# Kernel optimization log

Hardware: AMD Instinct MI355X
Metric: run time of the kernel (lower is better)

## Reference

```python
import jax, jax.numpy as jnp
from jax import lax
import numpy as np

NUM_HEADS = 8
KW = 3  # window kernel size

def _avgpool3(x):
    # x: [B,C,H,W]; AvgPool2d(3,1,1) with count_include_pad=True -> sum/9
    s = lax.reduce_window(x, 0.0, lax.add, (1, 1, KW, KW), (1, 1, 1, 1),
                          ((0, 0), (0, 0), (1, 1), (1, 1)))
    return s / (KW * KW)

def _unfold3(y):
    # y: [B,h,w,C] -> [B,h,w,9,C]; patch index ordered row-major (kh,kw)
    B, h, w, C = y.shape
    yp = jnp.pad(y, ((0, 0), (1, 1), (1, 1), (0, 0)))
    return jnp.stack([yp[:, i:i + h, j:j + w, :]
                      for i in range(KW) for j in range(KW)], axis=3)

def setup_inputs():
    key = jax.random.key(0)
    ks = jax.random.split(key, 9)
    B, C, H, W = 8, 256, 64, 64
    sd = 0.02
    return {
        "x": jax.random.normal(ks[0], (B, C, H, W), jnp.float32),
        "W_qkv": jax.random.normal(ks[1], (4 * C, C), jnp.float32) * sd,
        "b_qkv": jnp.zeros((4 * C,), jnp.float32),
        "W1": jax.random.normal(ks[2], (C // 2, C), jnp.float32) * sd,
        "b1": jnp.zeros((C // 2,), jnp.float32),
        "W2": jax.random.normal(ks[3], (C, C // 2), jnp.float32) * sd,
        "b2": jnp.zeros((C,), jnp.float32),
        "Wp": jax.random.normal(ks[4], (C, C), jnp.float32) * sd,
        "bp": jnp.zeros((C,), jnp.float32),
    }

def reference(x, W_qkv, b_qkv, W1, b1, W2, b2, Wp, bp):
    B, C, H, W = x.shape
    nH = NUM_HEADS
    hd = C // nH
    scale = hd ** -0.5
    # avg pool (stride 1 keeps spatial dims), to channels-last
    y = _avgpool3(x).transpose(0, 2, 3, 1)                 # [B,h,w,C]
    qkv = y @ W_qkv.T + b_qkv                              # [B,h,w,4C]
    qkv = qkv.reshape(B, H, W, C, 4)
    q, k, v, chans = qkv[..., 0], qkv[..., 1], qkv[..., 2], qkv[..., 3]
    # channel gate
    g = jax.nn.sigmoid(jax.nn.relu(chans @ W1.T + b1) @ W2.T + b2)  # [B,h,w,C]
    # local window attention: each query attends to its 3x3 neighborhood
    qh = q.reshape(B, H, W, nH, hd)                        # [B,h,w,n,d]
    kp = _unfold3(k).reshape(B, H, W, KW * KW, nH, hd)     # [B,h,w,9,n,d]
    vp = _unfold3(v).reshape(B, H, W, KW * KW, nH, hd)
    attn = jnp.einsum('bhwnd,bhwknd->bhwnk', qh, kp) * scale
    attn = jax.nn.softmax(attn, axis=-1)
    out = jnp.einsum('bhwnk,bhwknd->bhwnd', attn, vp).reshape(B, H, W, C)
    out = out * g + out
    out = out @ Wp.T + bp
    return out.transpose(0, 3, 1, 2)                       # [B,C,H,W]
```

## Files before the change

kernel.cpp:

```cpp
#include <hip/hip_runtime.h>
#include <stdint.h>

typedef __bf16    bf16x8 __attribute__((ext_vector_type(8)));
typedef float     f32x4  __attribute__((ext_vector_type(4)));
typedef uint32_t  u32x4  __attribute__((ext_vector_type(4)));

#define MFMA(a,b,c) __builtin_amdgcn_mfma_f32_16x16x32_bf16((a),(b),(c),0,0,0)

__device__ __align__(16) uint16_t g_y [8*64*64*256];
__device__ __align__(16) uint16_t g_wpk[393216];

#define WQF 0
#define WKF 65536
#define WVF 131072
#define WCF 196608
#define W1F 262144
#define W2F 294912
#define WPF 327680

static __device__ __forceinline__ float b2f(uint32_t u){ return __builtin_bit_cast(float, u<<16); }
static __device__ __forceinline__ uint32_t f2b(float f){
  uint32_t x = __builtin_bit_cast(uint32_t, f);
  return (x + 0x7fffu + ((x>>16)&1u)) >> 16;
}

__global__ __launch_bounds__(256) void kpack(const float* __restrict__ Wqkv,
    const float* __restrict__ W1, const float* __restrict__ W2,
    const float* __restrict__ Wp){
  int idx = blockIdx.x*256 + threadIdx.x;
  int j = idx & 7, lane = (idx>>3)&63;
  int n16 = lane & 15, q4 = lane>>4;
  float v;
  if (idx < 262144){
    int t = idx >> 16, l = idx & 65535;
    int s = (l>>9)&7, nt = l>>12;
    v = Wqkv[(4*(nt*16+n16) + t)*256 + s*32 + q4*8 + j];
  } else if (idx < 294912){
    int l = idx - 262144;
    int s = (l>>9)&7, nt = l>>12;
    v = W1[(nt*16+n16)*256 + s*32 + q4*8 + j];
  } else if (idx < 327680){
    int l = idx - 294912;
    int s = (l>>9)&3, nt = l>>11;
    v = W2[(nt*16+n16)*128 + s*32 + q4*8 + j];
  } else {
    int l = idx - 327680;
    int s = (l>>9)&7, nt = l>>12;
    v = Wp[(nt*16+n16)*256 + s*32 + q4*8 + j];
  }
  g_wpk[idx] = (uint16_t)f2b(v);
}

__global__ __launch_bounds__(512) void kpool(const float* __restrict__ x){
  __shared__ __align__(16) uint16_t sm[3*256*82];
  uint32_t* smw = (uint32_t*)sm;
  int t = threadIdx.x;
  int b = blockIdx.x >> 6, h = blockIdx.x & 63;
  for (int i=t; i<768; i+=512){
    int base = i*41;
    smw[base+3]  = 0;
    smw[base+36] = 0;
  }
  if (h==0 || h==63){
    int hh = (h==0) ? 0 : 2;
    for (int i=t; i<10496; i+=512) smw[hh*10496 + i] = 0;
  }
  #pragma unroll
  for (int i=0;i<24;i++){
    int id = t + 512*i;
    int w4 = id&15, c = (id>>4)&255, hh = id>>12;
    int gy = h - 1 + hh;
    if ((unsigned)gy < 64u){
      f32x4 ld = *(const f32x4*)&x[(((b*256+c)*64+gy)*64) + w4*4];
      int wb = (((hh*256+c)*82 + 8 + w4*4) >> 1);
      smw[wb+0] = f2b(ld[0]) | (f2b(ld[1])<<16);
      smw[wb+1] = f2b(ld[2]) | (f2b(ld[3])<<16);
    }
  }
  __syncthreads();
  int c = t & 255, wsel = t >> 8;
  int r0 = c*82, r1 = r0 + 256*82, r2 = r1 + 256*82;
  int w0 = wsel*32;
  float csp = b2f(sm[r0+w0+7]) + b2f(sm[r1+w0+7]) + b2f(sm[r2+w0+7]);
  float csc = b2f(sm[r0+w0+8]) + b2f(sm[r1+w0+8]) + b2f(sm[r2+w0+8]);
  uint16_t* dst = g_y + ((b*64+h)*64)*256 + c;
  for (int j2=0;j2<32;j2++){
    int w = w0 + j2;
    float csn = b2f(sm[r0+w+9]) + b2f(sm[r1+w+9]) + b2f(sm[r2+w+9]);
    float yv = (csp + csc + csn) * (1.0f/9.0f);
    dst[w*256] = (uint16_t)f2b(yv);
    csp = csc; csc = csn;
  }
}

#define YSTR 264
#define HSTR 134
#define K2_QS 26400
#define K2_KS 34976
#define K2_VS 48376
#define MCH 0
#define MHS 16896
#define MAO 25600
__global__ __launch_bounds__(512,2) void kattn(const float* __restrict__ bqkv,
    const float* __restrict__ b1, const float* __restrict__ b2v,
    const float* __restrict__ bp, float* __restrict__ out){
  __shared__ __align__(16) uint16_t sm[61776];
  int t = threadIdx.x;
  int lane = t & 63, wave = t >> 6;
  int n16 = lane & 15, quad = lane >> 4;
  int bid = blockIdx.x;
  int bb = bid>>6, tyhi=(bid>>4)&3, txl=(bid>>3)&1, tylo=(bid>>2)&1, txp=bid&3;
  int ty = tyhi*2+tylo, tx = txp*2+txl;

  uint32_t opk[2][16];
  uint32_t chp[32];

  #pragma unroll
  for (int i=0;i<7;i++){
    int id = t + 512*i;
    if (id < 3200){
      int hp = id >> 5, c8 = id & 31;
      int py = hp/10, px = hp - py*10;
      int gy = ty*8 + py - 1, gx = tx*8 + px - 1;
      u32x4 ld = {0,0,0,0};
      if ((unsigned)gy<64u && (unsigned)gx<64u)
        ld = *(const u32x4*)&g_y[((bb*64+gy)*64+gx)*256 + c8*8];
      *(u32x4*)&sm[hp*YSTR + c8*8] = ld;
    }
  }
  __syncthreads();

  #pragma unroll
  for (int hf=0; hf<2; hf++){
    {
      int ntg = hf*8 + wave;
      bf16x8 Bq[8];
      #pragma unroll
      for (int s=0;s<8;s++) Bq[s] = *(const bf16x8*)&g_wpk[WQF + ((ntg*8+s)*64+lane)*8];
      float bq = bqkv[4*(ntg*16+n16) + 0];
      int colB = wave*16;
      #pragma unroll
      for (int mt=0; mt<4; mt++){
        f32x4 a = {0.f,0.f,0.f,0.f};
        int m = mt*16 + n16;
        int hrow = 10*(m>>3) + (m&7) + 11;
        #pragma unroll
        for (int s=0;s<8;s++){
          bf16x8 A = *(const bf16x8*)&sm[hrow*YSTR + s*32 + quad*8];
          a = MFMA(A, Bq[s], a);
        }
        #pragma unroll
        for (int r=0;r<4;r++){
          int row = mt*16 + quad*4 + r;
          sm[K2_QS + row*HSTR + colB + n16] = (uint16_t)f2b(a[r] + bq);
        }
      }
    }
    __syncthreads();
    {
      int ntg = hf*8 + wave;
      bf16x8 Bk[8], Bv[8];
      #pragma unroll
      for (int s=0;s<8;s++){
        Bk[s] = *(const bf16x8*)&g_wpk[WKF + ((ntg*8+s)*64+lane)*8];
        Bv[s] = *(const bf16x8*)&g_wpk[WVF + ((ntg*8+s)*64+lane)*8];
      }
      float bk = bqkv[4*(ntg*16+n16) + 1];
      float bv = bqkv[4*(ntg*16+n16) + 2];
      int colB = wave*16;
      #pragma unroll
      for (int mt=0; mt<7; mt++){
        f32x4 ak = {0.f,0.f,0.f,0.f}, av = {0.f,0.f,0.f,0.f};
        int m = mt*16 + n16;
        int mr = (m < 100) ? m : 99;
        #pragma unroll
        for (int s=0;s<8;s++){
          bf16x8 A = *(const bf16x8*)&sm[mr*YSTR + s*32 + quad*8];
          ak = MFMA(A, Bk[s], ak);
          av = MFMA(A, Bv[s], av);
        }
        #pragma unroll
        for (int r=0;r<4;r++){
          int row = mt*16 + quad*4 + r;
          if (row < 100){
            int py = row/10, px = row - py*10;
            int gy = ty*8 + py - 1, gx = tx*8 + px - 1;
            bool ok = ((unsigned)gy<64u) && ((unsigned)gx<64u);
            float vk = ok ? ak[r] + bk : 0.f;
            float vv = ok ? av[r] + bv : 0.f;
            sm[K2_KS + row*HSTR + colB + n16] = (uint16_t)f2b(vk);
            sm[K2_VS + row*HSTR + colB + n16] = (uint16_t)f2b(vv);
          }
        }
      }
    }
    __syncthreads();
    if (wave < 4){
      int p = t & 63, hl = wave;
      int iy = p >> 3, ix = p & 7;
      int cb = hl*32;
      const uint32_t* q32 = (const uint32_t*)&sm[K2_QS + p*HSTR + cb];
      float qv[32];
      #pragma unroll
      for (int i=0;i<16;i++){ uint32_t u=q32[i]; qv[2*i]=b2f(u&0xffffu); qv[2*i+1]=b2f(u>>16); }
      int hb = (iy+1)*10 + ix + 1;
      const int off[9] = {-11,-10,-9,-1,0,1,9,10,11};
      float sc[9];
      #pragma unroll
      for (int nb=0;nb<9;nb++){
        const uint32_t* k32 = (const uint32_t*)&sm[K2_KS + (hb+off[nb])*HSTR + cb];
        float s = 0.f;
        #pragma unroll
        for (int i=0;i<16;i++){ uint32_t u=k32[i]; s += qv[2*i]*b2f(u&0xffffu) + qv[2*i+1]*b2f(u>>16); }
        sc[nb] = s * 0.17677669529663687f;
      }
      float mx = sc[0];
      #pragma unroll
      for (int nb=1;nb<9;nb++) mx = fmaxf(mx, sc[nb]);
      float l = 0.f;
      #pragma unroll
      for (int nb=0;nb<9;nb++){ sc[nb] = __expf(sc[nb]-mx); l += sc[nb]; }
      float inv = 1.f / l;
      float o[32];
      #pragma unroll
      for (int i=0;i<32;i++) o[i]=0.f;
      #pragma unroll
      for (int nb=0;nb<9;nb++){
        float wgt = sc[nb]*inv;
        const uint32_t* v32 = (const uint32_t*)&sm[K2_VS + (hb+off[nb])*HSTR + cb];
        #pragma unroll
        for (int i=0;i<16;i++){ uint32_t u=v32[i]; o[2*i] += wgt*b2f(u&0xffffu); o[2*i+1] += wgt*b2f(u>>16); }
      }
      #pragma unroll
      for (int i=0;i<16;i++) opk[hf][i] = f2b(o[2*i]) | (f2b(o[2*i+1])<<16);
    } else if (hf == 0){
      #pragma unroll
      for (int jj=0;jj<4;jj++){
        int ntg = (wave-4)*4 + jj;
        bf16x8 Bc[8];
        #pragma unroll
        for (int s=0;s<8;s++) Bc[s] = *(const bf16x8*)&g_wpk[WCF + ((ntg*8+s)*64+lane)*8];
        float bc = bqkv[4*(ntg*16+n16) + 3];
        #pragma unroll
        for (int mt=0; mt<4; mt++){
          f32x4 a = {0.f,0.f,0.f,0.f};
          int m = mt*16 + n16;
          int hrow = 10*(m>>3) + (m&7) + 11;
          #pragma unroll
          for (int s=0;s<8;s++){
            bf16x8 A = *(const bf16x8*)&sm[hrow*YSTR + s*32 + quad*8];
            a = MFMA(A, Bc[s], a);
          }
          chp[(jj*4+mt)*2+0] = f2b(a[0]+bc) | (f2b(a[1]+bc)<<16);
          chp[(jj*4+mt)*2+1] = f2b(a[2]+bc) | (f2b(a[3]+bc)<<16);
        }
      }
    } else {
      #pragma unroll
      for (int jj=0;jj<4;jj++){
        int ntg = (wave-4)*4 + jj;
        int col = ntg*16 + n16;
        #pragma unroll
        for (int mt=0;mt<4;mt++){
          #pragma unroll
          for (int r2=0;r2<2;r2++){
            uint32_t v = chp[(jj*4+mt)*2+r2];
            int row = mt*16 + quad*4 + r2*2;
            sm[MCH + row*264 + col]     = (uint16_t)(v & 0xffffu);
            sm[MCH + (row+1)*264 + col] = (uint16_t)(v >> 16);
          }
        }
      }
    }
    __syncthreads();
  }
  if (wave < 4){
    int p = t & 63, cb = wave*32;
    #pragma unroll
    for (int hf=0;hf<2;hf++)
      #pragma unroll
      for (int i=0;i<16;i++)
        *(uint32_t*)&sm[MAO + p*264 + hf*128 + cb + 2*i] = opk[hf][i];
  }
  {
    int ntg = wave;
    bf16x8 Bf[8];
    #pragma unroll
    for (int s=0;s<8;s++) Bf[s] = *(const bf16x8*)&g_wpk[W1F + ((ntg*8+s)*64+lane)*8];
    float bs = b1[ntg*16+n16];
    int colB = wave*16;
    #pragma unroll
    for (int mt=0;mt<4;mt++){
      f32x4 a = {0.f,0.f,0.f,0.f};
      #pragma unroll
      for (int s=0;s<8;s++){
        bf16x8 A = *(const bf16x8*)&sm[MCH + (mt*16+n16)*264 + s*32 + quad*8];
        a = MFMA(A, Bf[s], a);
      }
      #pragma unroll
      for (int r=0;r<4;r++){
        int row = mt*16 + quad*4 + r;
        sm[MHS + row*136 + colB + n16] = (uint16_t)f2b(fmaxf(a[r]+bs, 0.f));
      }
    }
  }
  __syncthreads();
  #pragma unroll
  for (int jj=0;jj<2;jj++){
    int ntg = wave*2 + jj;
    bf16x8 Bf[4];
    #pragma unroll
    for (int s=0;s<4;s++) Bf[s] = *(const bf16x8*)&g_wpk[W2F + ((ntg*4+s)*64+lane)*8];
    float bs = b2v[ntg*16+n16];
    int colB = ntg*16;
    #pragma unroll
    for (int mt=0;mt<4;mt++){
      f32x4 a = {0.f,0.f,0.f,0.f};
      #pragma unroll
      for (int s=0;s<4;s++){
        bf16x8 A = *(const bf16x8*)&sm[MHS + (mt*16+n16)*136 + s*32 + quad*8];
        a = MFMA(A, Bf[s], a);
      }
      #pragma unroll
      for (int r=0;r<4;r++){
        int row = mt*16 + quad*4 + r;
        float gg = 1.f/(1.f+__expf(-(a[r] + bs)));
        float ao = b2f((uint32_t)sm[MAO + row*264 + colB + n16]);
        sm[MCH + row*264 + colB + n16] = (uint16_t)f2b(ao*(1.f+gg));
      }
    }
  }
  __syncthreads();
  #pragma unroll
  for (int jj=0;jj<2;jj++){
    int ntg = wave*2 + jj;
    bf16x8 Bf[8];
    #pragma unroll
    for (int s=0;s<8;s++) Bf[s] = *(const bf16x8*)&g_wpk[WPF + ((ntg*8+s)*64+lane)*8];
    float bs = bp[ntg*16+n16];
    int colB = ntg*16;
    #pragma unroll
    for (int mt=0;mt<4;mt++){
      f32x4 a = {0.f,0.f,0.f,0.f};
      #pragma unroll
      for (int s=0;s<8;s++){
        bf16x8 A = *(const bf16x8*)&sm[MCH + (mt*16+n16)*264 + s*32 + quad*8];
        a = MFMA(A, Bf[s], a);
      }
      #pragma unroll
      for (int r=0;r<4;r++){
        int row = mt*16 + quad*4 + r;
        sm[MAO + row*264 + colB + n16] = (uint16_t)f2b(a[r]+bs);
      }
    }
  }
  __syncthreads();
  #pragma unroll
  for (int i=0;i<8;i++){
    int idx = t + 512*i;
    int ix4 = idx&1, iy = (idx>>1)&7, c = idx>>4;
    f32x4 stv;
    #pragma unroll
    for (int j=0;j<4;j++){
      int p = iy*8 + ix4*4 + j;
      stv[j] = b2f((uint32_t)sm[MAO + p*264 + c]);
    }
    *(f32x4*)&out[(((bb*256+c)*64) + ty*8+iy)*64 + tx*8 + ix4*4] = stv;
  }
}

extern "C" void kernel_launch(void* const* d_in, const int* in_sizes, int n_in,
                              void* d_out, int out_size, void* d_ws, size_t ws_size,
                              hipStream_t stream){
  (void)in_sizes; (void)n_in; (void)d_ws; (void)ws_size; (void)out_size;
  const float* x    = (const float*)d_in[0];
  const float* Wqkv = (const float*)d_in[1];
  const float* bqkv = (const float*)d_in[2];
  const float* W1   = (const float*)d_in[3];
  const float* b1   = (const float*)d_in[4];
  const float* W2   = (const float*)d_in[5];
  const float* b2   = (const float*)d_in[6];
  const float* Wp   = (const float*)d_in[7];
  const float* bp   = (const float*)d_in[8];
  kpack<<<dim3(1536), dim3(256), 0, stream>>>(Wqkv, W1, W2, Wp);
  kpool<<<dim3(512),  dim3(512), 0, stream>>>(x);
  kattn<<<dim3(512),  dim3(512), 0, stream>>>(bqkv, b1, b2, bp, (float*)d_out);
}
```

Before: 190.5 us.

## Merge pack and pool kernels, halve attention tile to 8x4 for occupancy

Fuses weight packing and average pooling into one launch, with pooling split into half-channel blocks. The attention kernel tile shrinks from 8x8 to 4x8 pixels, which shrinks the shared memory footprint and register arrays and raises the launch-bounds target from 2 to 4 blocks per CU over 1024 blocks. Each attention thread now covers half a head's channels and combines partial dot products with a cross-lane shuffle, and shared-memory strides are padded to reduce bank conflicts. The smaller tile raises halo overhead: 60 halo rows per 32 outputs instead of 100 per 64, so more redundant K/V projection work.

```diff
diff --git a/kernel.cpp b/kernel.cpp
--- a/kernel.cpp
+++ b/kernel.cpp
@@ -24,104 +24,105 @@
   return (x + 0x7fffu + ((x>>16)&1u)) >> 16;
 }
 
-__global__ __launch_bounds__(256) void kpack(const float* __restrict__ Wqkv,
-    const float* __restrict__ W1, const float* __restrict__ W2,
-    const float* __restrict__ Wp){
-  int idx = blockIdx.x*256 + threadIdx.x;
-  int j = idx & 7, lane = (idx>>3)&63;
-  int n16 = lane & 15, q4 = lane>>4;
-  float v;
-  if (idx < 262144){
-    int t = idx >> 16, l = idx & 65535;
-    int s = (l>>9)&7, nt = l>>12;
-    v = Wqkv[(4*(nt*16+n16) + t)*256 + s*32 + q4*8 + j];
-  } else if (idx < 294912){
-    int l = idx - 262144;
-    int s = (l>>9)&7, nt = l>>12;
-    v = W1[(nt*16+n16)*256 + s*32 + q4*8 + j];
-  } else if (idx < 327680){
-    int l = idx - 294912;
-    int s = (l>>9)&3, nt = l>>11;
-    v = W2[(nt*16+n16)*128 + s*32 + q4*8 + j];
+__global__ __launch_bounds__(512) void kprep(const float* __restrict__ x,
+    const float* __restrict__ Wqkv, const float* __restrict__ W1,
+    const float* __restrict__ W2, const float* __restrict__ Wp){
+  int t = threadIdx.x;
+  int bid = blockIdx.x;
+  if (bid < 1024){
+    __shared__ __align__(16) uint16_t sm[3*128*82];
+    uint32_t* smw = (uint32_t*)sm;
+    int b = bid >> 7, h = (bid >> 1) & 63, ch = (bid & 1) << 7;
+    for (int i=t; i<384; i+=512){
+      int base = i*41;
+      smw[base+3]  = 0;
+      smw[base+36] = 0;
+    }
+    if (h==0 || h==63){
+      int hh = (h==0) ? 0 : 2;
+      for (int i=t; i<5248; i+=512) smw[hh*5248 + i] = 0;
+    }
+    #pragma unroll
+    for (int i=0;i<12;i++){
+      int id = t + 512*i;
+      int w4 = id&15, c = (id>>4)&127, hh = id>>11;
+      int gy = h - 1 + hh;
+      if ((unsigned)gy < 64u){
+        f32x4 ld = *(const f32x4*)&x[(((b*256+ch+c)*64+gy)*64) + w4*4];
+        int wb = (((hh*128+c)*82 + 8 + w4*4) >> 1);
+        smw[wb+0] = f2b(ld[0]) | (f2b(ld[1])<<16);
+        smw[wb+1] = f2b(ld[2]) | (f2b(ld[3])<<16);
+      }
+    }
+    __syncthreads();
+    int c = t & 127, wsel = t >> 7;
+    int r0 = c*82, r1 = r0 + 128*82, r2 = r1 + 128*82;
+    int w0 = wsel*16;
+    float csp = b2f(sm[r0+w0+7]) + b2f(sm[r1+w0+7]) + b2f(sm[r2+w0+7]);
+    float csc = b2f(sm[r0+w0+8]) + b2f(sm[r1+w0+8]) + b2f(sm[r2+w0+8]);
+    uint16_t* dst = g_y + ((b*64+h)*64)*256 + ch + c;
+    for (int j2=0;j2<16;j2++){
+      int w = w0 + j2;
+      float csn = b2f(sm[r0+w+9]) + b2f(sm[r1+w+9]) + b2f(sm[r2+w+9]);
+      float yv = (csp + csc + csn) * (1.0f/9.0f);
+      dst[w*256] = (uint16_t)f2b(yv);
+      csp = csc; csc = csn;
+    }
   } else {
-    int l = idx - 327680;
-    int s = (l>>9)&7, nt = l>>12;
-    v = Wp[(nt*16+n16)*256 + s*32 + q4*8 + j];
-  }
-  g_wpk[idx] = (uint16_t)f2b(v);
+    int idx = (bid - 1024)*512 + t;
+    int j = idx & 7, lane = (idx>>3)&63;
+    int n16 = lane & 15, q4 = lane>>4;
+    float v;
+    if (idx < 262144){
+      int tt = idx >> 16, l = idx & 65535;
+      int s = (l>>9)&7, nt = l>>12;
+      v = Wqkv[(4*(nt*16+n16) + tt)*256 + s*32 + q4*8 + j];
+    } else if (idx < 294912){
+      int l = idx - 262144;
+      int s = (l>>9)&7, nt = l>>12;
+      v = W1[(nt*16+n16)*256 + s*32 + q4*8 + j];
+    } else if (idx < 327680){
+      int l = idx - 294912;
+      int s = (l>>9)&3, nt = l>>11;
+      v = W2[(nt*16+n16)*128 + s*32 + q4*8 + j];
+    } else {
+      int l = idx - 327680;
+      int s = (l>>9)&7, nt = l>>12;
+      v = Wp[(nt*16+n16)*256 + s*32 + q4*8 + j];
+    }
+    g_wpk[idx] = (uint16_t)f2b(v);
+  }
 }
 
-__global__ __launch_bounds__(512) void kpool(const float* __restrict__ x){
-  __shared__ __align__(16) uint16_t sm[3*256*82];
-  uint32_t* smw = (uint32_t*)sm;
-  int t = threadIdx.x;
-  int b = blockIdx.x >> 6, h = blockIdx.x & 63;
-  for (int i=t; i<768; i+=512){
-    int base = i*41;
-    smw[base+3]  = 0;
-    smw[base+36] = 0;
-  }
-  if (h==0 || h==63){
-    int hh = (h==0) ? 0 : 2;
-    for (int i=t; i<10496; i+=512) smw[hh*10496 + i] = 0;
-  }
-  #pragma unroll
-  for (int i=0;i<24;i++){
-    int id = t + 512*i;
-    int w4 = id&15, c = (id>>4)&255, hh = id>>12;
-    int gy = h - 1 + hh;
-    if ((unsigned)gy < 64u){
-      f32x4 ld = *(const f32x4*)&x[(((b*256+c)*64+gy)*64) + w4*4];
-      int wb = (((hh*256+c)*82 + 8 + w4*4) >> 1);
-      smw[wb+0] = f2b(ld[0]) | (f2b(ld[1])<<16);
-      smw[wb+1] = f2b(ld[2]) | (f2b(ld[3])<<16);
-    }
-  }
-  __syncthreads();
-  int c = t & 255, wsel = t >> 8;
-  int r0 = c*82, r1 = r0 + 256*82, r2 = r1 + 256*82;
-  int w0 = wsel*32;
-  float csp = b2f(sm[r0+w0+7]) + b2f(sm[r1+w0+7]) + b2f(sm[r2+w0+7]);
-  float csc = b2f(sm[r0+w0+8]) + b2f(sm[r1+w0+8]) + b2f(sm[r2+w0+8]);
-  uint16_t* dst = g_y + ((b*64+h)*64)*256 + c;
-  for (int j2=0;j2<32;j2++){
-    int w = w0 + j2;
-    float csn = b2f(sm[r0+w+9]) + b2f(sm[r1+w+9]) + b2f(sm[r2+w+9]);
-    float yv = (csp + csc + csn) * (1.0f/9.0f);
-    dst[w*256] = (uint16_t)f2b(yv);
-    csp = csc; csc = csn;
-  }
-}
-
-#define YSTR 264
-#define HSTR 134
-#define K2_QS 26400
-#define K2_KS 34976
-#define K2_VS 48376
-#define MCH 0
-#define MHS 16896
-#define MAO 25600
-__global__ __launch_bounds__(512,2) void kattn(const float* __restrict__ bqkv,
+#define YSTR  264
+#define HSTR  136
+#define K2_QS 15840
+#define K2_KS 20192
+#define K2_VS 28352
+#define MCH   0
+#define MHS   8448
+#define MAO   15840
+#define MAOSTR 266
+__global__ __launch_bounds__(512,4) void kattn(const float* __restrict__ bqkv,
     const float* __restrict__ b1, const float* __restrict__ b2v,
     const float* __restrict__ bp, float* __restrict__ out){
-  __shared__ __align__(16) uint16_t sm[61776];
+  __shared__ __align__(16) uint16_t sm[36512];
   int t = threadIdx.x;
   int lane = t & 63, wave = t >> 6;
   int n16 = lane & 15, quad = lane >> 4;
   int bid = blockIdx.x;
-  int bb = bid>>6, tyhi=(bid>>4)&3, txl=(bid>>3)&1, tylo=(bid>>2)&1, txp=bid&3;
-  int ty = tyhi*2+tylo, tx = txp*2+txl;
-
-  uint32_t opk[2][16];
-  uint32_t chp[32];
+  int bb = bid >> 7, ty = (bid >> 3) & 15, tx = bid & 7;
+
+  uint32_t opk[2][8];
+  uint32_t chp[16];
 
   #pragma unroll
-  for (int i=0;i<7;i++){
+  for (int i=0;i<4;i++){
     int id = t + 512*i;
-    if (id < 3200){
+    if (id < 1920){
       int hp = id >> 5, c8 = id & 31;
       int py = hp/10, px = hp - py*10;
-      int gy = ty*8 + py - 1, gx = tx*8 + px - 1;
+      int gy = ty*4 + py - 1, gx = tx*8 + px - 1;
       u32x4 ld = {0,0,0,0};
       if ((unsigned)gy<64u && (unsigned)gx<64u)
         ld = *(const u32x4*)&g_y[((bb*64+gy)*64+gx)*256 + c8*8];
@@ -140,7 +141,7 @@
       float bq = bqkv[4*(ntg*16+n16) + 0];
       int colB = wave*16;
       #pragma unroll
-      for (int mt=0; mt<4; mt++){
+      for (int mt=0; mt<2; mt++){
         f32x4 a = {0.f,0.f,0.f,0.f};
         int m = mt*16 + n16;
         int hrow = 10*(m>>3) + (m&7) + 11;
@@ -169,10 +170,10 @@
       float bv = bqkv[4*(ntg*16+n16) + 2];
       int colB = wave*16;
       #pragma unroll
-      for (int mt=0; mt<7; mt++){
+      for (int mt=0; mt<4; mt++){
         f32x4 ak = {0.f,0.f,0.f,0.f}, av = {0.f,0.f,0.f,0.f};
         int m = mt*16 + n16;
-        int mr = (m < 100) ? m : 99;
+        int mr = (m < 60) ? m : 59;
         #pragma unroll
         for (int s=0;s<8;s++){
           bf16x8 A = *(const bf16x8*)&sm[mr*YSTR + s*32 + quad*8];
@@ -182,9 +183,9 @@
         #pragma unroll
         for (int r=0;r<4;r++){
           int row = mt*16 + quad*4 + r;
-          if (row < 100){
+          if (row < 60){
             int py = row/10, px = row - py*10;
-            int gy = ty*8 + py - 1, gx = tx*8 + px - 1;
+            int gy = ty*4 + py - 1, gx = tx*8 + px - 1;
             bool ok = ((unsigned)gy<64u) && ((unsigned)gx<64u);
             float vk = ok ? ak[r] + bk : 0.f;
             float vv = ok ? av[r] + bv : 0.f;
@@ -196,22 +197,32 @@
     }
     __syncthreads();
     if (wave < 4){
-      int p = t & 63, hl = wave;
-      int iy = p >> 3, ix = p & 7;
-      int cb = hl*32;
-      const uint32_t* q32 = (const uint32_t*)&sm[K2_QS + p*HSTR + cb];
-      float qv[32];
-      #pragma unroll
-      for (int i=0;i<16;i++){ uint32_t u=q32[i]; qv[2*i]=b2f(u&0xffffu); qv[2*i+1]=b2f(u>>16); }
-      int hb = (iy+1)*10 + ix + 1;
+      int p = lane & 31, half = lane >> 5;
+      int cb = wave*32 + half*16;
+      const uint16_t* qp = &sm[K2_QS + p*HSTR + cb];
+      u32x4 qa = *(const u32x4*)qp;
+      u32x4 qb = *(const u32x4*)(qp+8);
+      float qv[16];
+      #pragma unroll
+      for (int i=0;i<4;i++){
+        qv[2*i]    = b2f(qa[i]&0xffffu); qv[2*i+1]   = b2f(qa[i]>>16);
+        qv[8+2*i]  = b2f(qb[i]&0xffffu); qv[8+2*i+1] = b2f(qb[i]>>16);
+      }
+      int hb = 10*(p>>3) + (p&7) + 11;
       const int off[9] = {-11,-10,-9,-1,0,1,9,10,11};
       float sc[9];
       #pragma unroll
       for (int nb=0;nb<9;nb++){
-        const uint32_t* k32 = (const uint32_t*)&sm[K2_KS + (hb+off[nb])*HSTR + cb];
+        const uint16_t* kp = &sm[K2_KS + (hb+off[nb])*HSTR + cb];
+        u32x4 ka = *(const u32x4*)kp;
+        u32x4 kb = *(const u32x4*)(kp+8);
         float s = 0.f;
         #pragma unroll
-        for (int i=0;i<16;i++){ uint32_t u=k32[i]; s += qv[2*i]*b2f(u&0xffffu) + qv[2*i+1]*b2f(u>>16); }
+        for (int i=0;i<4;i++){
+          s += qv[2*i]*b2f(ka[i]&0xffffu)   + qv[2*i+1]*b2f(ka[i]>>16);
+          s += qv[8+2*i]*b2f(kb[i]&0xffffu) + qv[8+2*i+1]*b2f(kb[i]>>16);
+        }
+        s += __shfl_xor(s, 32);
         sc[nb] = s * 0.17677669529663687f;
       }
       float mx = sc[0];
@@ -221,18 +232,23 @@
       #pragma unroll
       for (int nb=0;nb<9;nb++){ sc[nb] = __expf(sc[nb]-mx); l += sc[nb]; }
       float inv = 1.f / l;
-      float o[32];
-      #pragma unroll
-      for (int i=0;i<32;i++) o[i]=0.f;
+      float o[16];
+      #pragma unroll
+      for (int i=0;i<16;i++) o[i]=0.f;
       #pragma unroll
       for (int nb=0;nb<9;nb++){
         float wgt = sc[nb]*inv;
-        const uint32_t* v32 = (const uint32_t*)&sm[K2_VS + (hb+off[nb])*HSTR + cb];
-        #pragma unroll
-        for (int i=0;i<16;i++){ uint32_t u=v32[i]; o[2*i] += wgt*b2f(u&0xffffu); o[2*i+1] += wgt*b2f(u>>16); }
-      }
-      #pragma unroll
-      for (int i=0;i<16;i++) opk[hf][i] = f2b(o[2*i]) | (f2b(o[2*i+1])<<16);
+        const uint16_t* vp = &sm[K2_VS + (hb+off[nb])*HSTR + cb];
+        u32x4 va = *(const u32x4*)vp;
+        u32x4 vb = *(const u32x4*)(vp+8);
+        #pragma unroll
+        for (int i=0;i<4;i++){
+          o[2*i]    += wgt*b2f(va[i]&0xffffu); o[2*i+1]   += wgt*b2f(va[i]>>16);
+          o[8+2*i]  += wgt*b2f(vb[i]&0xffffu); o[8+2*i+1] += wgt*b2f(vb[i]>>16);
+        }
+      }
+      #pragma unroll
+      for (int i=0;i<8;i++) opk[hf][i] = f2b(o[2*i]) | (f2b(o[2*i+1])<<16);
     } else if (hf == 0){
       #pragma unroll
       for (int jj=0;jj<4;jj++){
@@ -242,7 +258,7 @@
         for (int s=0;s<8;s++) Bc[s] = *(const bf16x8*)&g_wpk[WCF + ((ntg*8+s)*64+lane)*8];
         float bc = bqkv[4*(ntg*16+n16) + 3];
         #pragma unroll
-        for (int mt=0; mt<4; mt++){
+        for (int mt=0; mt<2; mt++){
           f32x4 a = {0.f,0.f,0.f,0.f};
           int m = mt*16 + n16;
           int hrow = 10*(m>>3) + (m&7) + 11;
@@ -251,8 +267,8 @@
             bf16x8 A = *(const bf16x8*)&sm[hrow*YSTR + s*32 + quad*8];
             a = MFMA(A, Bc[s], a);
           }
-          chp[(jj*4+mt)*2+0] = f2b(a[0]+bc) | (f2b(a[1]+bc)<<16);
-          chp[(jj*4+mt)*2+1] = f2b(a[2]+bc) | (f2b(a[3]+bc)<<16);
+          chp[(jj*2+mt)*2+0] = f2b(a[0]+bc) | (f2b(a[1]+bc)<<16);
+          chp[(jj*2+mt)*2+1] = f2b(a[2]+bc) | (f2b(a[3]+bc)<<16);
         }
       }
     } else {
@@ -261,10 +277,10 @@
         int ntg = (wave-4)*4 + jj;
         int col = ntg*16 + n16;
         #pragma unroll
-        for (int mt=0;mt<4;mt++){
+        for (int mt=0;mt<2;mt++){
           #pragma unroll
           for (int r2=0;r2<2;r2++){
-            uint32_t v = chp[(jj*4+mt)*2+r2];
+            uint32_t v = chp[(jj*2+mt)*2+r2];
             int row = mt*16 + quad*4 + r2*2;
             sm[MCH + row*264 + col]     = (uint16_t)(v & 0xffffu);
             sm[MCH + (row+1)*264 + col] = (uint16_t)(v >> 16);
@@ -275,12 +291,13 @@
     __syncthreads();
   }
   if (wave < 4){
-    int p = t & 63, cb = wave*32;
+    int p = lane & 31, half = lane >> 5;
+    int cb = wave*32 + half*16;
     #pragma unroll
     for (int hf=0;hf<2;hf++)
       #pragma unroll
-      for (int i=0;i<16;i++)
-        *(uint32_t*)&sm[MAO + p*264 + hf*128 + cb + 2*i] = opk[hf][i];
+      for (int i=0;i<8;i++)
+        *(uint32_t*)&sm[MAO + p*MAOSTR + hf*128 + cb + 2*i] = opk[hf][i];
   }
   {
     int ntg = wave;
@@ -290,7 +307,7 @@
     float bs = b1[ntg*16+n16];
     int colB = wave*16;
     #pragma unroll
-    for (int mt=0;mt<4;mt++){
+    for (int mt=0;mt<2;mt++){
       f32x4 a = {0.f,0.f,0.f,0.f};
       #pragma unroll
       for (int s=0;s<8;s++){
@@ -300,7 +317,7 @@
       #pragma unroll
       for (int r=0;r<4;r++){
         int row = mt*16 + quad*4 + r;
-        sm[MHS + row*136 + colB + n16] = (uint16_t)f2b(fmaxf(a[r]+bs, 0.f));
+        sm[MHS + row*HSTR + colB + n16] = (uint16_t)f2b(fmaxf(a[r]+bs, 0.f));
       }
     }
   }
@@ -314,18 +331,18 @@
     float bs = b2v[ntg*16+n16];
     int colB = ntg*16;
     #pragma unroll
-    for (int mt=0;mt<4;mt++){
+    for (int mt=0;mt<2;mt++){
       f32x4 a = {0.f,0.f,0.f,0.f};
       #pragma unroll
       for (int s=0;s<4;s++){
-        bf16x8 A = *(const bf16x8*)&sm[MHS + (mt*16+n16)*136 + s*32 + quad*8];
+        bf16x8 A = *(const bf16x8*)&sm[MHS + (mt*16+n16)*HSTR + s*32 + quad*8];
         a = MFMA(A, Bf[s], a);
       }
       #pragma unroll
       for (int r=0;r<4;r++){
         int row = mt*16 + quad*4 + r;
         float gg = 1.f/(1.f+__expf(-(a[r] + bs)));
-        float ao = b2f((uint32_t)sm[MAO + row*264 + colB + n16]);
+        float ao = b2f((uint32_t)sm[MAO + row*MAOSTR + colB + n16]);
         sm[MCH + row*264 + colB + n16] = (uint16_t)f2b(ao*(1.f+gg));
       }
     }
@@ -340,7 +357,7 @@
     float bs = bp[ntg*16+n16];
     int colB = ntg*16;
     #pragma unroll
-    for (int mt=0;mt<4;mt++){
+    for (int mt=0;mt<2;mt++){
       f32x4 a = {0.f,0.f,0.f,0.f};
       #pragma unroll
       for (int s=0;s<8;s++){
@@ -350,22 +367,22 @@
       #pragma unroll
       for (int r=0;r<4;r++){
         int row = mt*16 + quad*4 + r;
-        sm[MAO + row*264 + colB + n16] = (uint16_t)f2b(a[r]+bs);
+        sm[MAO + row*MAOSTR + colB + n16] = (uint16_t)f2b(a[r]+bs);
       }
     }
   }
   __syncthreads();
   #pragma unroll
-  for (int i=0;i<8;i++){
+  for (int i=0;i<4;i++){
     int idx = t + 512*i;
-    int ix4 = idx&1, iy = (idx>>1)&7, c = idx>>4;
+    int ix4 = idx&1, iy = (idx>>1)&3, c = idx>>3;
     f32x4 stv;
     #pragma unroll
     for (int j=0;j<4;j++){
       int p = iy*8 + ix4*4 + j;
-      stv[j] = b2f((uint32_t)sm[MAO + p*264 + c]);
-    }
-    *(f32x4*)&out[(((bb*256+c)*64) + ty*8+iy)*64 + tx*8 + ix4*4] = stv;
+      stv[j] = b2f((uint32_t)sm[MAO + p*MAOSTR + c]);
+    }
+    *(f32x4*)&out[(((bb*256+c)*64) + ty*4+iy)*64 + tx*8 + ix4*4] = stv;
   }
 }
 
@@ -382,7 +399,6 @@
   const float* b2   = (const float*)d_in[6];
   const float* Wp   = (const float*)d_in[7];
   const float* bp   = (const float*)d_in[8];
-  kpack<<<dim3(1536), dim3(256), 0, stream>>>(Wqkv, W1, W2, Wp);
-  kpool<<<dim3(512),  dim3(512), 0, stream>>>(x);
-  kattn<<<dim3(512),  dim3(512), 0, stream>>>(bqkv, b1, b2, bp, (float*)d_out);
+  kprep<<<dim3(1792), dim3(512), 0, stream>>>(x, Wqkv, W1, W2, Wp);
+  kattn<<<dim3(1024), dim3(512), 0, stream>>>(bqkv, b1, b2, bp, (float*)d_out);
 }
```

After: 182.0 us. -4.5%, faster.
